# Kernel tuning notes

Hardware: AMD Instinct MI355X
Metric: run time of the kernel (lower is better)

## Reference

```python
import jax, jax.numpy as jnp
import numpy as np

# Transformer-XL relative multi-head attention (eval mode, dropout = identity)
B, Q, M, D, H = 2, 1024, 1024, 1024, 16
DH = D // H          # 64 head dim
K = Q + M            # key length = memory + current segment
SCALE = 0.02         # param init scale


def setup_inputs() -> dict:
    key = jax.random.key(0)
    ks = jax.random.split(key, 10)
    return {
        "inputs": jax.random.normal(ks[0], (B, Q, D), jnp.float32),
        "inputs_mem": jax.random.normal(ks[1], (B, M, D), jnp.float32),
        "r": jax.random.normal(ks[2], (B, K, D), jnp.float32),
        "W_qkv": jax.random.normal(ks[3], (D, 3 * D), jnp.float32) * SCALE,
        "b_qkv": jnp.zeros((3 * D,), jnp.float32),
        "W_r": jax.random.normal(ks[4], (D, D), jnp.float32) * SCALE,
        "b_r": jnp.zeros((D,), jnp.float32),
        "W_o": jax.random.normal(ks[5], (D, D), jnp.float32) * SCALE,
        "b_o": jnp.zeros((D,), jnp.float32),
        "u": jax.random.normal(ks[6], (1, H, 1, DH), jnp.float32) * SCALE,
        "v": jax.random.normal(ks[7], (1, H, 1, DH), jnp.float32) * SCALE,
    }


def _split_heads(x):
    # [B, L, D] -> [B, H, L, DH]
    b, l, _ = x.shape
    return x.reshape(b, l, H, DH).transpose(0, 2, 1, 3)


def _rel_shift(x):
    # Transformer-XL relative shift: pad one zero column on the left,
    # reshape to [B, H, K+1, Q], drop first row, reshape back.
    b, h, q, k = x.shape
    x = jnp.pad(x, ((0, 0), (0, 0), (0, 0), (1, 0)))
    x = x.reshape(b, h, k + 1, q)[:, :, 1:, :]
    return x.reshape(b, h, q, k)


def reference(inputs, inputs_mem, r, W_qkv, b_qkv, W_r, b_r, W_o, b_o, u, v):
    cat = jnp.concatenate([inputs_mem, inputs], axis=1)      # [B, K, D]
    w = cat @ W_qkv + b_qkv                                   # [B, K, 3D]
    rp = r @ W_r + b_r                                        # [B, K, D]
    # NOTE: source splits as (q, v, k) in that order
    w_q, w_v, w_k = jnp.split(w, 3, axis=-1)
    hq = _split_heads(w_q)[:, :, -Q:]                          # [B, H, Q, DH]
    hk = _split_heads(w_k)                                     # [B, H, K, DH]
    hv = _split_heads(w_v)                                     # [B, H, K, DH]
    hr = _split_heads(rp)                                      # [B, H, K, DH]
    ac = jnp.einsum('bhqd,bhkd->bhqk', hq + u, hk)             # content term
    bd = _rel_shift(jnp.einsum('bhqd,bhkd->bhqk', hq + v, hr)) # position term
    score = (ac + bd) / (DH ** 0.5)
    # causal mask with memory: query i attends to all mem + positions <= i
    mem_len = K - Q
    mask = (jnp.arange(K)[None, :] <= mem_len + jnp.arange(Q)[:, None]).astype(jnp.float32)
    score = score * mask - 1e30 * (1.0 - mask)
    weights = jax.nn.softmax(score, axis=-1)                   # [B, H, Q, K]
    out = jnp.einsum('bhqk,bhkd->bhqd', weights, hv)           # [B, H, Q, DH]
    out = out.transpose(0, 2, 1, 3).reshape(B, Q, D)
    return out @ W_o + b_o
```

## Files before the change

kernel.cpp:

```cpp
#include <hip/hip_runtime.h>
#include <hip/hip_bf16.h>
#include <stdint.h>


typedef __bf16 bf16;
typedef __bf16 bf16x2 __attribute__((ext_vector_type(2)));
typedef __bf16 bf16x4 __attribute__((ext_vector_type(4)));
typedef __bf16 bf16x8 __attribute__((ext_vector_type(8)));
typedef float  f32x4  __attribute__((ext_vector_type(4)));

__device__ __forceinline__ void async_copy16(void* lds, const void* g) {
    auto gp = (const __attribute__((address_space(1))) void*)(uintptr_t)g;
    auto lp = (__attribute__((address_space(3))) void*)(uint32_t)(uintptr_t)lds;
    __builtin_amdgcn_global_load_lds(gp, lp, 16, 0, 0);
}

__device__ __forceinline__ void gemm128_core(
    const bf16* __restrict__ A, const bf16* __restrict__ Bt, const int Kd,
    const int m0, const int n0, bf16* As, bf16* Bs, f32x4 acc[4][4])
{
    const int tid  = threadIdx.x;
    const int lane = tid & 63;
    const int wave = tid >> 6;
    const int wr   = (wave >> 1) * 64;
    const int wc   = (wave & 1) * 64;
    const int lr   = lane & 15;
    const int q4   = lane >> 4;

#pragma unroll
    for (int i = 0; i < 4; ++i)
#pragma unroll
        for (int j = 0; j < 4; ++j) {
            acc[i][j][0] = 0.f; acc[i][j][1] = 0.f; acc[i][j][2] = 0.f; acc[i][j][3] = 0.f;
        }

    for (int k0 = 0; k0 < Kd; k0 += 32) {
#pragma unroll
        for (int it = 0; it < 2; ++it) {
            const int cb0   = (it * 4 + wave) * 64;
            const int chunk = cb0 + lane;
            const int row   = chunk >> 2;
            const int cg    = (chunk & 3) * 8;
            async_copy16(As + cb0 * 8, A  + (size_t)(m0 + row) * Kd + k0 + cg);
            async_copy16(Bs + cb0 * 8, Bt + (size_t)(n0 + row) * Kd + k0 + cg);
        }
        __syncthreads();
        bf16x8 af[4], bfr[4];
#pragma unroll
        for (int rb = 0; rb < 4; ++rb)
            af[rb] = *(const bf16x8*)&As[(wr + rb * 16 + lr) * 32 + q4 * 8];
#pragma unroll
        for (int cb = 0; cb < 4; ++cb)
            bfr[cb] = *(const bf16x8*)&Bs[(wc + cb * 16 + lr) * 32 + q4 * 8];
#pragma unroll
        for (int rb = 0; rb < 4; ++rb)
#pragma unroll
            for (int cb = 0; cb < 4; ++cb)
                acc[rb][cb] = __builtin_amdgcn_mfma_f32_16x16x32_bf16(af[rb], bfr[cb], acc[rb][cb], 0, 0, 0);
        __syncthreads();
    }
}

__global__ __launch_bounds__(256) void k_tcast(const float* __restrict__ in,
                                               bf16* __restrict__ out, int R, int C)
{
    __shared__ float t[32][33];
    const int c0 = blockIdx.x * 32, r0 = blockIdx.y * 32;
    const int lc = threadIdx.x & 31, lrow = threadIdx.x >> 5;
#pragma unroll
    for (int p = 0; p < 4; ++p)
        t[lrow + p * 8][lc] = in[(size_t)(r0 + lrow + p * 8) * C + c0 + lc];
    __syncthreads();
#pragma unroll
    for (int p = 0; p < 4; ++p)
        out[(size_t)(c0 + lrow + p * 8) * R + r0 + lc] = (bf16)t[lc][lrow + p * 8];
}

__global__ __launch_bounds__(256) void k_cast_cat(const float* __restrict__ mem,
                                                  const float* __restrict__ inp,
                                                  bf16* __restrict__ catb)
{
    const int e   = (blockIdx.x * 256 + threadIdx.x) * 4;
    const int row = e >> 10, dc = e & 1023;
    const int b   = row >> 11, k = row & 2047;
    const float* src = (k < 1024) ? mem + ((size_t)b * 1024 + k) * 1024 + dc
                                  : inp + ((size_t)b * 1024 + (k - 1024)) * 1024 + dc;
    float4 f = *(const float4*)src;
    bf16x4 o; o[0] = (bf16)f.x; o[1] = (bf16)f.y; o[2] = (bf16)f.z; o[3] = (bf16)f.w;
    *(bf16x4*)&catb[e] = o;
}

__global__ __launch_bounds__(256) void k_cast(const float* __restrict__ in,
                                              bf16* __restrict__ out)
{
    const int e = (blockIdx.x * 256 + threadIdx.x) * 4;
    float4 f = *(const float4*)(in + e);
    bf16x4 o; o[0] = (bf16)f.x; o[1] = (bf16)f.y; o[2] = (bf16)f.z; o[3] = (bf16)f.w;
    *(bf16x4*)&out[e] = o;
}

__global__ __launch_bounds__(256) void k_gemm_qkvr(
    const bf16* __restrict__ catb, const bf16* __restrict__ Wqkvt,
    const float* __restrict__ b_qkv, const float* __restrict__ u, const float* __restrict__ v,
    const bf16* __restrict__ rb_, const bf16* __restrict__ Wrt,
    const float* __restrict__ b_r,
    bf16* __restrict__ hq_u, bf16* __restrict__ hq_v,
    bf16* __restrict__ hk, bf16* __restrict__ hvT, bf16* __restrict__ hr)
{
    __shared__ bf16 lds[2 * 128 * 32];
    f32x4 acc[4][4];
    const int m0 = blockIdx.x * 128;
    const int lane = threadIdx.x & 63, wave = threadIdx.x >> 6;
    const int wr = (wave >> 1) * 64, wc = (wave & 1) * 64;
    const int lr = lane & 15, q4 = lane >> 4;

    if (blockIdx.y < 24) {
        const int n0 = blockIdx.y * 128;
        gemm128_core(catb, Wqkvt, 1024, m0, n0, lds, lds + 128 * 32, acc);
#pragma unroll
        for (int rb = 0; rb < 4; ++rb) {
#pragma unroll
            for (int cb = 0; cb < 4; ++cb) {
                const int col  = n0 + wc + cb * 16 + lr;
                const int part = col >> 10;
                const int hd   = col & 1023;
                const int h    = hd >> 6, d = hd & 63;
                const float bcol = b_qkv[col];
#pragma unroll
                for (int r = 0; r < 4; ++r) {
                    const int row = m0 + wr + rb * 16 + q4 * 4 + r;
                    const int b   = row >> 11, k = row & 2047;
                    const float val = acc[rb][cb][r] + bcol;
                    if (part == 0) {
                        if (k >= 1024) {
                            const size_t o = (((size_t)(b * 16 + h)) * 1024 + (k - 1024)) * 64 + d;
                            hq_u[o] = (bf16)(val + u[hd]);
                            hq_v[o] = (bf16)(val + v[hd]);
                        }
                    } else if (part == 1) {
                        hvT[(((size_t)(b * 16 + h)) * 64 + d) * 2048 + k] = (bf16)val;
                    } else {
                        hk[(((size_t)(b * 16 + h)) * 2048 + k) * 64 + d] = (bf16)val;
                    }
                }
            }
        }
    } else {
        const int n0 = (blockIdx.y - 24) * 128;
        gemm128_core(rb_, Wrt, 1024, m0, n0, lds, lds + 128 * 32, acc);
#pragma unroll
        for (int rb = 0; rb < 4; ++rb) {
#pragma unroll
            for (int cb = 0; cb < 4; ++cb) {
                const int col = n0 + wc + cb * 16 + lr;
                const int h = col >> 6, d = col & 63;
                const float bcol = b_r[col];
#pragma unroll
                for (int r = 0; r < 4; ++r) {
                    const int row = m0 + wr + rb * 16 + q4 * 4 + r;
                    const int b = row >> 11, k = row & 2047;
                    hr[(((size_t)(b * 16 + h)) * 2048 + k) * 64 + d] = (bf16)(acc[rb][cb][r] + bcol);
                }
            }
        }
    }
}

__global__ __launch_bounds__(256) void k_gemm_out(
    const bf16* __restrict__ attn, const bf16* __restrict__ Wt,
    const float* __restrict__ bias, float* __restrict__ out)
{
    __shared__ bf16 lds[2 * 128 * 32];
    f32x4 acc[4][4];
    const int m0 = blockIdx.x * 128, n0 = blockIdx.y * 128;
    gemm128_core(attn, Wt, 1024, m0, n0, lds, lds + 128 * 32, acc);

    const int lane = threadIdx.x & 63, wave = threadIdx.x >> 6;
    const int wr = (wave >> 1) * 64, wc = (wave & 1) * 64;
    const int lr = lane & 15, q4 = lane >> 4;
#pragma unroll
    for (int rb = 0; rb < 4; ++rb) {
#pragma unroll
        for (int cb = 0; cb < 4; ++cb) {
            const int col = n0 + wc + cb * 16 + lr;
            const float bcol = bias[col];
#pragma unroll
            for (int r = 0; r < 4; ++r) {
                const int row = m0 + wr + rb * 16 + q4 * 4 + r;
                out[(size_t)row * 1024 + col] = acc[rb][cb][r] + bcol;
            }
        }
    }
}

__global__ __launch_bounds__(256) void k_attn(
    const bf16* __restrict__ hq_u, const bf16* __restrict__ hq_v,
    const bf16* __restrict__ hk, const bf16* __restrict__ hvT,
    const bf16* __restrict__ hr, bf16* __restrict__ attn)
{
    __shared__ bf16 Ks[2][64][72];
    __shared__ bf16 Vt[2][64][72];
    __shared__ bf16 Rs[192 * 72];
    __shared__ bf16 U[4][1344];

    const int bh = blockIdx.y;
    const int qt = (bh & 16) ? (15 - (int)blockIdx.x) : (int)blockIdx.x;
    const int q0 = qt * 64;
    const int tid = threadIdx.x, lane = tid & 63, wave = tid >> 6;
    const int lr = lane & 15, q4 = lane >> 4;
    bf16* Uw = &U[wave][0];

    const int nt  = 17 + qt;
    const int m0c = 15 - qt;
    const size_t kvbase = (size_t)bh * 2048 * 64;

    const int ci0  = tid,        r0_ = ci0 >> 3,  c0_ = (ci0 & 7) * 8;
    const int ci1  = 256 + tid,  r1_ = ci1 >> 3,  c1_ = (ci1 & 7) * 8;

    bf16x8 kv0, kv1, vv0, vv1, rv0, rv1;
    auto load_kv = [&](int t) {
        const int k0 = t * 64;
        kv0 = *(const bf16x8*)&hk [kvbase + (size_t)(k0 + r0_) * 64 + c0_];
        kv1 = *(const bf16x8*)&hk [kvbase + (size_t)(k0 + r1_) * 64 + c1_];
        vv0 = *(const bf16x8*)&hvT[kvbase + (size_t)r0_ * 2048 + k0 + c0_];
        vv1 = *(const bf16x8*)&hvT[kvbase + (size_t)r1_ * 2048 + k0 + c1_];
    };
    auto load_r = [&](int c) {
        if (c * 64 < 2048) {
            rv0 = *(const bf16x8*)&hr[kvbase + (size_t)(c * 64 + r0_) * 64 + c0_];
            rv1 = *(const bf16x8*)&hr[kvbase + (size_t)(c * 64 + r1_) * 64 + c1_];
        } else {
#pragma unroll
            for (int z = 0; z < 8; ++z) { rv0[z] = (bf16)0.f; rv1[z] = (bf16)0.f; }
        }
    };
    auto write_kv = [&](int buf) {
        *(bf16x8*)&Ks[buf][r0_][c0_] = kv0;
        *(bf16x8*)&Ks[buf][r1_][c1_] = kv1;
        *(bf16x8*)&Vt[buf][r0_][c0_] = vv0;
        *(bf16x8*)&Vt[buf][r1_][c1_] = vv1;
    };
    auto write_r = [&](int slot) {
        *(bf16x8*)&Rs[(slot * 64 + r0_) * 72 + c0_] = rv0;
        *(bf16x8*)&Rs[(slot * 64 + r1_) * 72 + c1_] = rv1;
    };

    const size_t qrow = ((size_t)bh * 1024 + q0 + wave * 16 + lr) * 64;
    const bf16x8 qu0 = *(const bf16x8*)&hq_u[qrow + q4 * 8];
    const bf16x8 qu1 = *(const bf16x8*)&hq_u[qrow + 32 + q4 * 8];
    const bf16x8 qv0 = *(const bf16x8*)&hq_v[qrow + q4 * 8];
    const bf16x8 qv1 = *(const bf16x8*)&hq_v[qrow + 32 + q4 * 8];

    f32x4 Oacc[4];
#pragma unroll
    for (int i = 0; i < 4; ++i) { Oacc[i][0] = 0.f; Oacc[i][1] = 0.f; Oacc[i][2] = 0.f; Oacc[i][3] = 0.f; }
    float lp[4] = {0.f, 0.f, 0.f, 0.f};

    load_kv(0);  write_kv(0);
    load_r(m0c);     write_r(m0c % 3);
    load_r(m0c + 1); write_r((m0c + 1) % 3);
    __syncthreads();

    for (int t = 0; t < nt; ++t) {
        const int k0  = t * 64;
        const int mt  = m0c + t;
        const int s0  = mt % 3;
        const int s1  = (s0 + 1 == 3) ? 0 : s0 + 1;
        const int s2  = (s1 + 1 == 3) ? 0 : s1 + 1;
        const int buf = t & 1;
        const bool more = (t + 1 < nt);
        if (more) { load_kv(t + 1); load_r(mt + 2); }

        __builtin_amdgcn_s_setprio(1);
        f32x4 S[4];
#pragma unroll
        for (int cb = 0; cb < 4; ++cb) {
            const bf16x8 kf0 = *(const bf16x8*)&Ks[buf][cb * 16 + lr][q4 * 8];
            const bf16x8 kf1 = *(const bf16x8*)&Ks[buf][cb * 16 + lr][32 + q4 * 8];
            f32x4 z; z[0] = 0.f; z[1] = 0.f; z[2] = 0.f; z[3] = 0.f;
            z = __builtin_amdgcn_mfma_f32_16x16x32_bf16(qu0, kf0, z, 0, 0, 0);
            S[cb] = __builtin_amdgcn_mfma_f32_16x16x32_bf16(qu1, kf1, z, 0, 0, 0);
        }
#pragma unroll
        for (int jbi = 0; jbi < 5; ++jbi) {
            const int jb   = jbi + 3 - wave;
            const int rrow = ((jb & 4) ? s1 : s0) * 64 + (jb & 3) * 16 + lr;
            const bf16x8 rf0 = *(const bf16x8*)&Rs[rrow * 72 + q4 * 8];
            const bf16x8 rf1 = *(const bf16x8*)&Rs[rrow * 72 + 32 + q4 * 8];
            f32x4 z; z[0] = 0.f; z[1] = 0.f; z[2] = 0.f; z[3] = 0.f;
            z = __builtin_amdgcn_mfma_f32_16x16x32_bf16(qv0, rf0, z, 0, 0, 0);
            z = __builtin_amdgcn_mfma_f32_16x16x32_bf16(qv1, rf1, z, 0, 0, 0);
#pragma unroll
            for (int r = 0; r < 4; ++r) Uw[(q4 * 4 + r) * 84 + jbi * 16 + lr] = (bf16)z[r];
        }

        float bdv[4][4];
#pragma unroll
        for (int cb = 0; cb < 4; ++cb)
#pragma unroll
            for (int r = 0; r < 4; ++r) {
                const int tq = q4 * 4 + r;
                bdv[cb][r] = (float)Uw[tq * 84 + cb * 16 + lr + 15 - tq];
            }

#pragma unroll
        for (int cb = 0; cb < 4; ++cb) {
            const int k = k0 + cb * 16 + lr;
#pragma unroll
            for (int r = 0; r < 4; ++r) {
                const int q = q0 + wave * 16 + q4 * 4 + r;
                const float s = (S[cb][r] + bdv[cb][r]) * 0.125f;
                const float p = (k <= 1024 + q) ? __expf(s) : 0.f;
                lp[r] += p;
                Uw[(q4 * 4 + r) * 76 + cb * 16 + lr] = (bf16)p;
            }
        }

        const bf16x8 pf0 = *(const bf16x8*)&Uw[lr * 76 + q4 * 8];
        const bf16x8 pf1 = *(const bf16x8*)&Uw[lr * 76 + 32 + q4 * 8];
#pragma unroll
        for (int db = 0; db < 4; ++db) {
            const bf16x8 vf0 = *(const bf16x8*)&Vt[buf][db * 16 + lr][q4 * 8];
            const bf16x8 vf1 = *(const bf16x8*)&Vt[buf][db * 16 + lr][32 + q4 * 8];
            Oacc[db] = __builtin_amdgcn_mfma_f32_16x16x32_bf16(pf0, vf0, Oacc[db], 0, 0, 0);
            Oacc[db] = __builtin_amdgcn_mfma_f32_16x16x32_bf16(pf1, vf1, Oacc[db], 0, 0, 0);
        }
        __builtin_amdgcn_s_setprio(0);

        if (more) {
            write_kv(buf ^ 1);
            write_r(s2);
            __syncthreads();
        }
    }

#pragma unroll
    for (int off = 1; off < 16; off <<= 1)
#pragma unroll
        for (int r = 0; r < 4; ++r) lp[r] += __shfl_xor(lp[r], off, 64);

    const int b = bh >> 4, h = bh & 15;
#pragma unroll
    for (int r = 0; r < 4; ++r) {
        const float rl = 1.f / lp[r];
        const int q = q0 + wave * 16 + q4 * 4 + r;
#pragma unroll
        for (int db = 0; db < 4; ++db) {
            const int d = db * 16 + lr;
            attn[(((size_t)b * 1024 + q) * 16 + h) * 64 + d] = (bf16)(Oacc[db][r] * rl);
        }
    }
}

extern "C" void kernel_launch(void* const* d_in, const int* in_sizes, int n_in,
                              void* d_out, int out_size, void* d_ws, size_t ws_size,
                              hipStream_t stream)
{
    const float* inputs = (const float*)d_in[0];
    const float* mem    = (const float*)d_in[1];
    const float* r      = (const float*)d_in[2];
    const float* W_qkv  = (const float*)d_in[3];
    const float* b_qkv  = (const float*)d_in[4];
    const float* W_r    = (const float*)d_in[5];
    const float* b_r    = (const float*)d_in[6];
    const float* W_o    = (const float*)d_in[7];
    const float* b_o    = (const float*)d_in[8];
    const float* u      = (const float*)d_in[9];
    const float* v      = (const float*)d_in[10];
    float* out = (float*)d_out;

    char* ws = (char*)d_ws;
    size_t off = 0;
    auto alloc = [&](size_t bytes) -> void* {
        void* p = ws + off;
        off += (bytes + 255) & ~(size_t)255;
        return p;
    };
    bf16* hq_u  = (bf16*)alloc(2ull * 16 * 1024 * 64 * 2);
    bf16* hq_v  = (bf16*)alloc(2ull * 16 * 1024 * 64 * 2);
    bf16* hk    = (bf16*)alloc(2ull * 16 * 2048 * 64 * 2);
    bf16* hvT   = (bf16*)alloc(2ull * 16 * 2048 * 64 * 2);
    bf16* hr    = (bf16*)alloc(2ull * 16 * 2048 * 64 * 2);
    bf16* attnb = (bf16*)alloc(2ull * 1024 * 1024 * 2);
    bf16* Wot   = (bf16*)alloc(1024ull * 1024 * 2);
    bf16* catb  = (bf16*)alloc(4096ull * 1024 * 2);
    bf16* rb    = (bf16*)alloc(4096ull * 1024 * 2);
    bf16* Wqkvt = (bf16*)alloc(3072ull * 1024 * 2);
    bf16* Wrt   = (bf16*)alloc(1024ull * 1024 * 2);

    k_tcast<<<dim3(96, 32), 256, 0, stream>>>(W_qkv, Wqkvt, 1024, 3072);
    k_tcast<<<dim3(32, 32), 256, 0, stream>>>(W_r, Wrt, 1024, 1024);
    k_tcast<<<dim3(32, 32), 256, 0, stream>>>(W_o, Wot, 1024, 1024);
    k_cast_cat<<<4096, 256, 0, stream>>>(mem, inputs, catb);
    k_cast<<<4096, 256, 0, stream>>>(r, rb);

    k_gemm_qkvr<<<dim3(32, 32), 256, 0, stream>>>(catb, Wqkvt, b_qkv, u, v,
                                                  rb, Wrt, b_r,
                                                  hq_u, hq_v, hk, hvT, hr);
    k_attn<<<dim3(16, 32), 256, 0, stream>>>(hq_u, hq_v, hk, hvT, hr, attnb);
    k_gemm_out<<<dim3(16, 8), 256, 0, stream>>>(attnb, Wot, b_o, out);
}
```

Before: 272.3 us.

## Load K, V and R fragments straight from global into registers, dropping LDS staging

The attention kernel no longer stages K, V^T and R tiles in shared memory behind per-iteration barriers. Each wave now loads its MFMA operand fragments directly from global memory into registers, with the next K tile prefetched one iteration ahead. Launch bounds now request two blocks per CU. This removes LDS writes, LDS reads and __syncthreads, but each of the four waves re-reads the same K/V tiles, which raises L1/L2 traffic. It also drops the zero-fill guard on R rows past 2048, so R reads can run past the head's range (possibly past the end of the buffer for the last head).

```diff
diff --git a/kernel.cpp b/kernel.cpp
--- a/kernel.cpp
+++ b/kernel.cpp
@@ -193,14 +193,11 @@
     }
 }
 
-__global__ __launch_bounds__(256) void k_attn(
+__global__ __launch_bounds__(256, 2) void k_attn(
     const bf16* __restrict__ hq_u, const bf16* __restrict__ hq_v,
     const bf16* __restrict__ hk, const bf16* __restrict__ hvT,
     const bf16* __restrict__ hr, bf16* __restrict__ attn)
 {
-    __shared__ bf16 Ks[2][64][72];
-    __shared__ bf16 Vt[2][64][72];
-    __shared__ bf16 Rs[192 * 72];
     __shared__ bf16 U[4][1344];
 
     const int bh = blockIdx.y;
@@ -210,40 +207,14 @@
     const int lr = lane & 15, q4 = lane >> 4;
     bf16* Uw = &U[wave][0];
 
-    const int nt  = 17 + qt;
-    const int m0c = 15 - qt;
+    const int nt    = 17 + qt;
+    const int m0c   = 15 - qt;
+    const int jbase = 3 - wave;
     const size_t kvbase = (size_t)bh * 2048 * 64;
 
-    const int ci0  = tid,        r0_ = ci0 >> 3,  c0_ = (ci0 & 7) * 8;
-    const int ci1  = 256 + tid,  r1_ = ci1 >> 3,  c1_ = (ci1 & 7) * 8;
-
-    bf16x8 kv0, kv1, vv0, vv1, rv0, rv1;
-    auto load_kv = [&](int t) {
-        const int k0 = t * 64;
-        kv0 = *(const bf16x8*)&hk [kvbase + (size_t)(k0 + r0_) * 64 + c0_];
-        kv1 = *(const bf16x8*)&hk [kvbase + (size_t)(k0 + r1_) * 64 + c1_];
-        vv0 = *(const bf16x8*)&hvT[kvbase + (size_t)r0_ * 2048 + k0 + c0_];
-        vv1 = *(const bf16x8*)&hvT[kvbase + (size_t)r1_ * 2048 + k0 + c1_];
-    };
-    auto load_r = [&](int c) {
-        if (c * 64 < 2048) {
-            rv0 = *(const bf16x8*)&hr[kvbase + (size_t)(c * 64 + r0_) * 64 + c0_];
-            rv1 = *(const bf16x8*)&hr[kvbase + (size_t)(c * 64 + r1_) * 64 + c1_];
-        } else {
-#pragma unroll
-            for (int z = 0; z < 8; ++z) { rv0[z] = (bf16)0.f; rv1[z] = (bf16)0.f; }
-        }
-    };
-    auto write_kv = [&](int buf) {
-        *(bf16x8*)&Ks[buf][r0_][c0_] = kv0;
-        *(bf16x8*)&Ks[buf][r1_][c1_] = kv1;
-        *(bf16x8*)&Vt[buf][r0_][c0_] = vv0;
-        *(bf16x8*)&Vt[buf][r1_][c1_] = vv1;
-    };
-    auto write_r = [&](int slot) {
-        *(bf16x8*)&Rs[(slot * 64 + r0_) * 72 + c0_] = rv0;
-        *(bf16x8*)&Rs[(slot * 64 + r1_) * 72 + c1_] = rv1;
-    };
+    const bf16* Kp = hk  + kvbase + (size_t)lr * 64   + q4 * 8;
+    const bf16* Vp = hvT + kvbase + (size_t)lr * 2048 + q4 * 8;
+    const bf16* Rp = hr  + kvbase + (size_t)lr * 64   + q4 * 8;
 
     const size_t qrow = ((size_t)bh * 1024 + q0 + wave * 16 + lr) * 64;
     const bf16x8 qu0 = *(const bf16x8*)&hq_u[qrow + q4 * 8];
@@ -256,40 +227,53 @@
     for (int i = 0; i < 4; ++i) { Oacc[i][0] = 0.f; Oacc[i][1] = 0.f; Oacc[i][2] = 0.f; Oacc[i][3] = 0.f; }
     float lp[4] = {0.f, 0.f, 0.f, 0.f};
 
-    load_kv(0);  write_kv(0);
-    load_r(m0c);     write_r(m0c % 3);
-    load_r(m0c + 1); write_r((m0c + 1) % 3);
-    __syncthreads();
+    bf16x8 ka[4][2];
+#pragma unroll
+    for (int cb = 0; cb < 4; ++cb) {
+        ka[cb][0] = *(const bf16x8*)(Kp + (size_t)(cb * 16) * 64);
+        ka[cb][1] = *(const bf16x8*)(Kp + (size_t)(cb * 16) * 64 + 32);
+    }
 
     for (int t = 0; t < nt; ++t) {
-        const int k0  = t * 64;
-        const int mt  = m0c + t;
-        const int s0  = mt % 3;
-        const int s1  = (s0 + 1 == 3) ? 0 : s0 + 1;
-        const int s2  = (s1 + 1 == 3) ? 0 : s1 + 1;
-        const int buf = t & 1;
+        const int k0 = t * 64;
+        const int mt = m0c + t;
         const bool more = (t + 1 < nt);
-        if (more) { load_kv(t + 1); load_r(mt + 2); }
+
+        bf16x8 ra[5][2];
+#pragma unroll
+        for (int jbi = 0; jbi < 5; ++jbi) {
+            const size_t rrow = (size_t)(mt * 64 + (jbase + jbi) * 16) * 64;
+            ra[jbi][0] = *(const bf16x8*)(Rp + rrow);
+            ra[jbi][1] = *(const bf16x8*)(Rp + rrow + 32);
+        }
+        bf16x8 va[4][2];
+#pragma unroll
+        for (int db = 0; db < 4; ++db) {
+            va[db][0] = *(const bf16x8*)(Vp + (size_t)(db * 16) * 2048 + k0);
+            va[db][1] = *(const bf16x8*)(Vp + (size_t)(db * 16) * 2048 + k0 + 32);
+        }
+        bf16x8 kn[4][2];
+        if (more) {
+#pragma unroll
+            for (int cb = 0; cb < 4; ++cb) {
+                kn[cb][0] = *(const bf16x8*)(Kp + (size_t)(k0 + 64 + cb * 16) * 64);
+                kn[cb][1] = *(const bf16x8*)(Kp + (size_t)(k0 + 64 + cb * 16) * 64 + 32);
+            }
+        }
 
         __builtin_amdgcn_s_setprio(1);
         f32x4 S[4];
 #pragma unroll
         for (int cb = 0; cb < 4; ++cb) {
-            const bf16x8 kf0 = *(const bf16x8*)&Ks[buf][cb * 16 + lr][q4 * 8];
-            const bf16x8 kf1 = *(const bf16x8*)&Ks[buf][cb * 16 + lr][32 + q4 * 8];
             f32x4 z; z[0] = 0.f; z[1] = 0.f; z[2] = 0.f; z[3] = 0.f;
-            z = __builtin_amdgcn_mfma_f32_16x16x32_bf16(qu0, kf0, z, 0, 0, 0);
-            S[cb] = __builtin_amdgcn_mfma_f32_16x16x32_bf16(qu1, kf1, z, 0, 0, 0);
+            z = __builtin_amdgcn_mfma_f32_16x16x32_bf16(qu0, ka[cb][0], z, 0, 0, 0);
+            S[cb] = __builtin_amdgcn_mfma_f32_16x16x32_bf16(qu1, ka[cb][1], z, 0, 0, 0);
         }
 #pragma unroll
         for (int jbi = 0; jbi < 5; ++jbi) {
-            const int jb   = jbi + 3 - wave;
-            const int rrow = ((jb & 4) ? s1 : s0) * 64 + (jb & 3) * 16 + lr;
-            const bf16x8 rf0 = *(const bf16x8*)&Rs[rrow * 72 + q4 * 8];
-            const bf16x8 rf1 = *(const bf16x8*)&Rs[rrow * 72 + 32 + q4 * 8];
             f32x4 z; z[0] = 0.f; z[1] = 0.f; z[2] = 0.f; z[3] = 0.f;
-            z = __builtin_amdgcn_mfma_f32_16x16x32_bf16(qv0, rf0, z, 0, 0, 0);
-            z = __builtin_amdgcn_mfma_f32_16x16x32_bf16(qv1, rf1, z, 0, 0, 0);
+            z = __builtin_amdgcn_mfma_f32_16x16x32_bf16(qv0, ra[jbi][0], z, 0, 0, 0);
+            z = __builtin_amdgcn_mfma_f32_16x16x32_bf16(qv1, ra[jbi][1], z, 0, 0, 0);
 #pragma unroll
             for (int r = 0; r < 4; ++r) Uw[(q4 * 4 + r) * 84 + jbi * 16 + lr] = (bf16)z[r];
         }
@@ -320,17 +304,17 @@
         const bf16x8 pf1 = *(const bf16x8*)&Uw[lr * 76 + 32 + q4 * 8];
 #pragma unroll
         for (int db = 0; db < 4; ++db) {
-            const bf16x8 vf0 = *(const bf16x8*)&Vt[buf][db * 16 + lr][q4 * 8];
-            const bf16x8 vf1 = *(const bf16x8*)&Vt[buf][db * 16 + lr][32 + q4 * 8];
-            Oacc[db] = __builtin_amdgcn_mfma_f32_16x16x32_bf16(pf0, vf0, Oacc[db], 0, 0, 0);
-            Oacc[db] = __builtin_amdgcn_mfma_f32_16x16x32_bf16(pf1, vf1, Oacc[db], 0, 0, 0);
+            Oacc[db] = __builtin_amdgcn_mfma_f32_16x16x32_bf16(pf0, va[db][0], Oacc[db], 0, 0, 0);
+            Oacc[db] = __builtin_amdgcn_mfma_f32_16x16x32_bf16(pf1, va[db][1], Oacc[db], 0, 0, 0);
         }
         __builtin_amdgcn_s_setprio(0);
 
         if (more) {
-            write_kv(buf ^ 1);
-            write_r(s2);
-            __syncthreads();
+#pragma unroll
+            for (int cb = 0; cb < 4; ++cb) {
+                ka[cb][0] = kn[cb][0];
+                ka[cb][1] = kn[cb][1];
+            }
         }
     }
 
```

New measurement: 339.2 us. 1.25x slower.
